# Kernel optimization log

Measured on AMD Instinct MI355X. Metric: run time of the kernel, lower is better.

The kernel has to match this reference:

```python
import jax, jax.numpy as jnp
import numpy as np

N_NODES = 100000
N_EDGES = 1600000
FEAT = 128
EMB = 128
N_ROOTS = 4096


def _gcn_layer(x, W, b, src, dst, n):
    # PyG GCNConv(add_self_loops=False, normalize=False):
    # h = x @ W; out_i = sum_{j in N(i)} h_j ; out = out + bias
    h = x @ W                                  # [N_in, EMB]
    msgs = h[src]                              # gather per edge [E, EMB]
    return jax.ops.segment_sum(msgs, dst, num_segments=n) + b


def setup_inputs() -> dict:
    key = jax.random.key(0)
    k = jax.random.split(key, 10)
    x = jax.random.normal(k[0], (N_NODES, FEAT), dtype=jnp.float32)
    edge_index = jax.random.randint(k[1], (2, N_EDGES), 0, N_NODES, dtype=jnp.int64 if jax.config.jax_enable_x64 else jnp.int32)
    root_mask = jnp.zeros((N_NODES,), dtype=bool).at[:N_ROOTS].set(True)
    s0 = 1.0 / np.sqrt(FEAT)
    s1 = 1.0 / np.sqrt(FEAT + EMB)
    W0 = jax.random.normal(k[2], (FEAT, EMB), dtype=jnp.float32) * s0
    W1 = jax.random.normal(k[3], (EMB + FEAT, EMB), dtype=jnp.float32) * s1
    W2 = jax.random.normal(k[4], (EMB + FEAT, EMB), dtype=jnp.float32) * s1
    W3 = jax.random.normal(k[5], (EMB + FEAT, EMB), dtype=jnp.float32) * s1
    b0 = jnp.zeros((EMB,), jnp.float32)
    b1 = jnp.zeros((EMB,), jnp.float32)
    b2 = jnp.zeros((EMB,), jnp.float32)
    b3 = jnp.zeros((EMB,), jnp.float32)
    return {"x": x, "edge_index": edge_index, "root_mask": root_mask, "num_roots": N_ROOTS,
            "W0": W0, "b0": b0, "W1": W1, "b1": b1, "W2": W2, "b2": b2, "W3": W3, "b3": b3}


def reference(x, edge_index, root_mask, num_roots, W0, b0, W1, b1, W2, b2, W3, b3):
    src, dst = edge_index[0], edge_index[1]
    n = x.shape[0]
    h = _gcn_layer(x, W0, b0, src, dst, n)
    for W, b in ((W1, b1), (W2, b2), (W3, b3)):
        prev = h
        inp = jnp.concatenate((jax.nn.relu(h), x), axis=1)  # concat_initial_features
        h = prev + _gcn_layer(inp, W, b, src, dst, n)        # residual
    roots = jnp.nonzero(root_mask, size=num_roots)[0]
    return h[roots]
```

## Files before the change

kernel.cpp:

```cpp
#include <hip/hip_runtime.h>
#include <hip/hip_bf16.h>
#include <stdint.h>

#define N_NODES 100000
#define N_EDGES 1600000
#define FEAT 128
#define EMB 128
#define N_ROOTS 4096

#define BUCKET_BITS 9
#define BUCKET_NODES 512
#define NBUCK ((N_NODES + BUCKET_NODES - 1) / BUCKET_NODES)
#define BUCK_CAP 12288
#define BIN_CHUNK 4096
#define NB_BIN ((N_EDGES + BIN_CHUNK - 1) / BIN_CHUNK)
#define SRCS_CAP (N_EDGES + N_NODES * 8)

typedef __attribute__((ext_vector_type(4))) float f32x4;
typedef __attribute__((ext_vector_type(8))) short bf16x8;

__device__ __forceinline__ ushort f2b(float f) {
  uint32_t u = __float_as_uint(f);
  uint32_t r = (u + 0x7FFFu + ((u >> 16) & 1u)) >> 16;
  return (ushort)r;
}

__global__ void k_cvt_bf16(const float* __restrict__ in, ushort* __restrict__ out, int n4) {
  int i = blockIdx.x * blockDim.x + threadIdx.x;
  int stride = gridDim.x * blockDim.x;
  for (; i < n4; i += stride) {
    float4 v = ((const float4*)in)[i];
    ushort4 o;
    o.x = f2b(v.x); o.y = f2b(v.y); o.z = f2b(v.z); o.w = f2b(v.w);
    ((ushort4*)out)[i] = o;
  }
}

__global__ __launch_bounds__(256) void k_bin(const int* __restrict__ srcA, const int* __restrict__ dstA,
                                             int* __restrict__ bucket_cnt, int* __restrict__ binned) {
  __shared__ int hist[NBUCK];
  __shared__ int lscan[NBUCK];
  __shared__ int rsv[NBUCK];
  __shared__ int lpos[NBUCK];
  __shared__ int ws[4];
  __shared__ int2 ent[BIN_CHUNK];
  int t = threadIdx.x;
  int e0 = blockIdx.x * BIN_CHUNK;
  int cnt = min(BIN_CHUNK, N_EDGES - e0);
  for (int i = t; i < NBUCK; i += 256) hist[i] = 0;
  __syncthreads();
  for (int j = t; j < cnt; j += 256) atomicAdd(&hist[dstA[e0 + j] >> BUCKET_BITS], 1);
  __syncthreads();
  {
    int lane = t & 63, wv = t >> 6;
    int v = (t < NBUCK) ? hist[t] : 0;
    int inc = v;
    for (int d = 1; d < 64; d <<= 1) { int x = __shfl_up(inc, d); if (lane >= d) inc += x; }
    if (lane == 63) ws[wv] = inc;
    __syncthreads();
    int wbase = 0;
    for (int k = 0; k < wv; ++k) wbase += ws[k];
    if (t < NBUCK) {
      int excl = wbase + inc - v;
      lscan[t] = excl;
      lpos[t] = excl;
      rsv[t] = (v > 0) ? atomicAdd(&bucket_cnt[t], v) : 0;
    }
  }
  __syncthreads();
  for (int j = t; j < cnt; j += 256) {
    int s = srcA[e0 + j], d = dstA[e0 + j];
    int p = atomicAdd(&lpos[d >> BUCKET_BITS], 1);
    ent[p] = make_int2(s, d);
  }
  __syncthreads();
  for (int j = t; j < cnt; j += 256) {
    int2 E = ent[j];
    int b = E.y >> BUCKET_BITS;
    int pos = rsv[b] + (j - lscan[b]);
    if (pos < BUCK_CAP)
      binned[b * BUCK_CAP + pos] = (E.x << BUCKET_BITS) | (E.y & (BUCKET_NODES - 1));
  }
}

__global__ __launch_bounds__(512) void k_deg(const int* __restrict__ binned,
                                             const int* __restrict__ bucket_cnt,
                                             int* __restrict__ degg, int* __restrict__ pad_cnt) {
  __shared__ int deg[BUCKET_NODES];
  __shared__ int ws[8];
  int b = blockIdx.x, t = threadIdx.x;
  int cnt = min(bucket_cnt[b], BUCK_CAP);
  deg[t] = 0;
  __syncthreads();
  for (int j = t; j < cnt; j += 512) atomicAdd(&deg[binned[b * BUCK_CAP + j] & (BUCKET_NODES - 1)], 1);
  __syncthreads();
  int n0 = b * BUCKET_NODES;
  int nn = min(BUCKET_NODES, N_NODES - n0);
  int d = (t < nn) ? deg[t] : 0;
  if (t < nn) degg[n0 + t] = d;
  int dp = (d + 7) & ~7;
  int lane = t & 63, wv = t >> 6;
  for (int q = 1; q < 64; q <<= 1) dp += __shfl_xor(dp, q);
  if (lane == 0) ws[wv] = dp;
  __syncthreads();
  if (t == 0) {
    int tot = 0;
    for (int k = 0; k < 8; ++k) tot += ws[k];
    pad_cnt[b] = tot;
  }
}

__global__ __launch_bounds__(256) void k_bucket_scan(const int* __restrict__ pad_cnt,
                                                     int* __restrict__ bucket_base,
                                                     int* __restrict__ off_last) {
  __shared__ int ws[4];
  int t = threadIdx.x;
  int lane = t & 63, wv = t >> 6;
  int v = (t < NBUCK) ? pad_cnt[t] : 0;
  int inc = v;
  for (int d = 1; d < 64; d <<= 1) { int x = __shfl_up(inc, d); if (lane >= d) inc += x; }
  if (lane == 63) ws[wv] = inc;
  __syncthreads();
  int wbase = 0;
  for (int k = 0; k < wv; ++k) wbase += ws[k];
  if (t < NBUCK) bucket_base[t] = wbase + inc - v;
  if (t == NBUCK - 1) *off_last = wbase + inc;
}

__global__ __launch_bounds__(512) void k_csr(const int* __restrict__ binned,
                                             const int* __restrict__ bucket_cnt,
                                             const int* __restrict__ bucket_base,
                                             const int* __restrict__ degg,
                                             int* __restrict__ off, int* __restrict__ srcs) {
  __shared__ int sAb[BUCKET_NODES];
  __shared__ int sBb[BUCKET_NODES];
  __shared__ int pos[BUCKET_NODES];
  __shared__ int dreal[BUCKET_NODES];
  __shared__ int epk[BUCK_CAP];
  int b = blockIdx.x;
  int t = threadIdx.x;
  int cnt = min(bucket_cnt[b], BUCK_CAP);
  int gbase = bucket_base[b];
  int n0 = b * BUCKET_NODES;
  int nn = min(BUCKET_NODES, N_NODES - n0);
  int d = (t < nn) ? degg[n0 + t] : 0;
  dreal[t] = d;
  int dp = (d + 7) & ~7;
  int* sA = sAb; int* sB = sBb;
  sA[t] = dp;
  __syncthreads();
  for (int q = 1; q < 512; q <<= 1) {
    int x = sA[t];
    if (t >= q) x += sA[t - q];
    sB[t] = x;
    __syncthreads();
    int* tp = sA; sA = sB; sB = tp;
  }
  int ex = sA[t] - dp;
  pos[t] = ex;
  if (t < nn) off[n0 + t] = gbase + ex;
  __syncthreads();
  for (int j = t; j < cnt; j += 512) {
    int p = binned[b * BUCK_CAP + j];
    epk[j] = p;
  }
  __syncthreads();
  for (int j = t; j < cnt; j += 512) {
    int p = epk[j];
    int q = atomicAdd(&pos[p & (BUCKET_NODES - 1)], 1);
    srcs[gbase + q] = p >> BUCKET_BITS;
  }
  __syncthreads();
  int start = sA[t] - dp;
  int fill0 = start + dreal[t];
  int fill1 = start + ((dreal[t] + 7) & ~7);
  for (int q = fill0; q < fill1; ++q) srcs[gbase + q] = N_NODES;
}

__global__ __launch_bounds__(256) void k_gemm(
    const ushort* __restrict__ A0, const ushort* __restrict__ A1,
    const float* __restrict__ W, ushort* __restrict__ out, int n, int K, int relu0)
{
  extern __shared__ char smem[];
  const int KC = K * 128;
  for (int idx = threadIdx.x; idx < KC; idx += 256) {
    int k = idx >> 7, c = idx & 127;
    ushort b = f2b(W[idx]);
    *(ushort*)(smem + c * (K * 2) + ((k * 2) ^ ((c & 7) << 4))) = b;
  }
  __syncthreads();

  int lane = threadIdx.x & 63;
  int wv = threadIdx.x >> 6;
  int rowBase = blockIdx.x * 128 + wv * 32;
  int rl = lane & 15;
  int kh = lane >> 4;
  int r0 = rowBase + rl, r1 = r0 + 16;
  int r0c = min(r0, n - 1), r1c = min(r1, n - 1);

  f32x4 acc[2][8];
#pragma unroll
  for (int i = 0; i < 2; ++i)
#pragma unroll
    for (int j = 0; j < 8; ++j)
      acc[i][j] = (f32x4){0.f, 0.f, 0.f, 0.f};

  int nks = K >> 5;
  for (int ks = 0; ks < nks; ++ks) {
    const ushort* Asrc = (ks < 4) ? A0 : A1;
    int kof = ((ks & 3) << 5) + (kh << 3);
    bf16x8 a0 = *(const bf16x8*)(Asrc + (size_t)r0c * 128 + kof);
    bf16x8 a1 = *(const bf16x8*)(Asrc + (size_t)r1c * 128 + kof);
    if (relu0 && ks < 4) {
#pragma unroll
      for (int q = 0; q < 8; ++q) {
        short v0 = a0[q]; a0[q] = (short)(v0 & ~(v0 >> 15));
        short v1 = a1[q]; a1[q] = (short)(v1 & ~(v1 >> 15));
      }
    }
    int kk = (ks << 5) + (kh << 3);
#pragma unroll
    for (int ct = 0; ct < 8; ++ct) {
      int col = (ct << 4) + rl;
      bf16x8 b = *(const bf16x8*)(smem + col * (K * 2) + ((kk * 2) ^ ((col & 7) << 4)));
      acc[0][ct] = __builtin_amdgcn_mfma_f32_16x16x32_bf16(a0, b, acc[0][ct], 0, 0, 0);
      acc[1][ct] = __builtin_amdgcn_mfma_f32_16x16x32_bf16(a1, b, acc[1][ct], 0, 0, 0);
    }
  }
#pragma unroll
  for (int ri = 0; ri < 2; ++ri)
#pragma unroll
    for (int ct = 0; ct < 8; ++ct) {
      int col = (ct << 4) + rl;
#pragma unroll
      for (int j = 0; j < 4; ++j) {
        int row = rowBase + ri * 16 + kh * 4 + j;
        if (row < n) out[(size_t)row * 128 + col] = f2b(acc[ri][ct][j]);
      }
    }
}

__global__ __launch_bounds__(256) void k_aggr(
    const ushort* __restrict__ hlin, const int* __restrict__ off, const int* __restrict__ srcs,
    const float* __restrict__ bias, ushort* __restrict__ hbf, float* __restrict__ outf,
    int n, int first, int last)
{
  int node = blockIdx.x * 4 + (threadIdx.x >> 6);
  if (node >= n) return;
  int lane = threadIdx.x & 63;
  int s = __builtin_amdgcn_readfirstlane(off[node]);
  int e = __builtin_amdgcn_readfirstlane(off[node + 1]);
  float a0 = 0.f, a1 = 0.f;
  int j = s;
  for (; j + 16 <= e; j += 16) {
    int ix[16];
#pragma unroll
    for (int q = 0; q < 16; ++q) ix[q] = srcs[j + q];
    uint32_t u[16];
#pragma unroll
    for (int q = 0; q < 16; ++q)
      u[q] = *(const uint32_t*)(hlin + (size_t)ix[q] * 128 + lane * 2);
#pragma unroll
    for (int q = 0; q < 16; ++q) {
      a0 += __uint_as_float(u[q] << 16);
      a1 += __uint_as_float(u[q] & 0xFFFF0000u);
    }
  }
  if (j < e) {
    int ix[8];
#pragma unroll
    for (int q = 0; q < 8; ++q) ix[q] = srcs[j + q];
    uint32_t u[8];
#pragma unroll
    for (int q = 0; q < 8; ++q)
      u[q] = *(const uint32_t*)(hlin + (size_t)ix[q] * 128 + lane * 2);
#pragma unroll
    for (int q = 0; q < 8; ++q) {
      a0 += __uint_as_float(u[q] << 16);
      a1 += __uint_as_float(u[q] & 0xFFFF0000u);
    }
  }
  float2 bv = ((const float2*)bias)[lane];
  size_t idx = (size_t)node * 128 + lane * 2;
  float h0, h1;
  if (first) {
    h0 = a0 + bv.x; h1 = a1 + bv.y;
  } else {
    uint32_t up = *(const uint32_t*)(hbf + idx);
    h0 = __uint_as_float(up << 16) + a0 + bv.x;
    h1 = __uint_as_float(up & 0xFFFF0000u) + a1 + bv.y;
  }
  if (last) {
    if (node < N_ROOTS) *(float2*)(outf + idx) = make_float2(h0, h1);
  } else {
    ushort2 r; r.x = f2b(h0); r.y = f2b(h1);
    *(ushort2*)(hbf + idx) = r;
  }
}

extern "C" void kernel_launch(void* const* d_in, const int* in_sizes, int n_in,
                              void* d_out, int out_size, void* d_ws, size_t ws_size,
                              hipStream_t stream) {
  const float* x = (const float*)d_in[0];
  const int* ei  = (const int*)d_in[1];
  const int* src = ei;
  const int* dst = ei + N_EDGES;
  const float* Wp[4] = {(const float*)d_in[4], (const float*)d_in[6],
                        (const float*)d_in[8], (const float*)d_in[10]};
  const float* bp[4] = {(const float*)d_in[5], (const float*)d_in[7],
                        (const float*)d_in[9], (const float*)d_in[11]};

  char* w = (char*)d_ws;
  auto alloc = [&](size_t bytes) {
    char* p = w;
    w += (bytes + 255) & ~(size_t)255;
    return p;
  };
  ushort* x_bf     = (ushort*)alloc((size_t)N_NODES * 128 * 2);
  ushort* hbf      = (ushort*)alloc((size_t)N_NODES * 128 * 2);
  ushort* hlin     = (ushort*)alloc((size_t)(N_NODES + 8) * 128 * 2);
  int*    off      = (int*)   alloc((size_t)(N_NODES + 1) * 4);
  int*    srcs     = (int*)   alloc((size_t)SRCS_CAP * 4);
  int*    binned   = (int*)   alloc((size_t)NBUCK * BUCK_CAP * 4);
  int*    degg     = (int*)   alloc((size_t)N_NODES * 4);
  int*    bucket_cnt  = (int*)alloc((size_t)NBUCK * 4);
  int*    pad_cnt     = (int*)alloc((size_t)NBUCK * 4);
  int*    bucket_base = (int*)alloc((size_t)(NBUCK + 1) * 4);
  if ((size_t)(w - (char*)d_ws) > ws_size) return;

  hipMemsetAsync(bucket_cnt, 0, (size_t)NBUCK * 4, stream);
  hipMemsetAsync(hlin + (size_t)N_NODES * 128, 0, 256, stream);
  k_cvt_bf16<<<2048, 256, 0, stream>>>(x, x_bf, N_NODES * 128 / 4);
  k_bin<<<NB_BIN, 256, 0, stream>>>(src, dst, bucket_cnt, binned);
  k_deg<<<NBUCK, 512, 0, stream>>>(binned, bucket_cnt, degg, pad_cnt);
  k_bucket_scan<<<1, 256, 0, stream>>>(pad_cnt, bucket_base, off + N_NODES);
  k_csr<<<NBUCK, 512, 0, stream>>>(binned, bucket_cnt, bucket_base, degg, off, srcs);

  int gblocks = (N_NODES + 127) / 128;
  int ablocks = (N_NODES + 3) / 4;
  k_gemm<<<gblocks, 256, 128 * 128 * 2, stream>>>(x_bf, x_bf, Wp[0], hlin, N_NODES, 128, 0);
  k_aggr<<<ablocks, 256, 0, stream>>>(hlin, off, srcs, bp[0], hbf, (float*)d_out, N_NODES, 1, 0);
  for (int l = 1; l < 4; ++l) {
    k_gemm<<<gblocks, 256, 256 * 128 * 2, stream>>>(hbf, x_bf, Wp[l], hlin, N_NODES, 256, 1);
    k_aggr<<<ablocks, 256, 0, stream>>>(hlin, off, srcs, bp[l], hbf, (float*)d_out,
                                        N_NODES, 0, (l == 3) ? 1 : 0);
  }
}
```

Before: 403.4 us.

## Slice node features into column slabs and map aggregation slices to XCDs

```diff
diff --git a/kernel.cpp b/kernel.cpp
--- a/kernel.cpp
+++ b/kernel.cpp
@@ -3,10 +3,8 @@
 #include <stdint.h>
 
 #define N_NODES 100000
+#define N_ROOTS 4096
 #define N_EDGES 1600000
-#define FEAT 128
-#define EMB 128
-#define N_ROOTS 4096
 
 #define BUCKET_BITS 9
 #define BUCKET_NODES 512
@@ -14,7 +12,10 @@
 #define BUCK_CAP 12288
 #define BIN_CHUNK 4096
 #define NB_BIN ((N_EDGES + BIN_CHUNK - 1) / BIN_CHUNK)
-#define SRCS_CAP (N_EDGES + N_NODES * 8)
+#define SRCS_CAP (N_EDGES + N_NODES * 8 + 256)
+
+#define ROWSP (N_NODES + 8)
+#define SLABW ((size_t)ROWSP * 32)
 
 typedef __attribute__((ext_vector_type(4))) float f32x4;
 typedef __attribute__((ext_vector_type(8))) short bf16x8;
@@ -25,14 +26,20 @@
   return (ushort)r;
 }
 
-__global__ void k_cvt_bf16(const float* __restrict__ in, ushort* __restrict__ out, int n4) {
-  int i = blockIdx.x * blockDim.x + threadIdx.x;
+__global__ void k_cvt_sliced(const float* __restrict__ in, ushort* __restrict__ out, int n) {
+  int g = blockIdx.x * blockDim.x + threadIdx.x;
   int stride = gridDim.x * blockDim.x;
-  for (; i < n4; i += stride) {
-    float4 v = ((const float4*)in)[i];
-    ushort4 o;
-    o.x = f2b(v.x); o.y = f2b(v.y); o.z = f2b(v.z); o.w = f2b(v.w);
-    ((ushort4*)out)[i] = o;
+  int total = n * 16;
+  for (; g < total; g += stride) {
+    int node = g >> 4, cg = g & 15;
+    const float4* p = (const float4*)(in + (size_t)node * 128 + cg * 8);
+    float4 v0 = p[0], v1 = p[1];
+    uint32_t w0 = (uint32_t)f2b(v0.x) | ((uint32_t)f2b(v0.y) << 16);
+    uint32_t w1 = (uint32_t)f2b(v0.z) | ((uint32_t)f2b(v0.w) << 16);
+    uint32_t w2 = (uint32_t)f2b(v1.x) | ((uint32_t)f2b(v1.y) << 16);
+    uint32_t w3 = (uint32_t)f2b(v1.z) | ((uint32_t)f2b(v1.w) << 16);
+    int slab = cg >> 2, in8 = (cg & 3) * 8;
+    *(uint4*)(out + (size_t)slab * SLABW + (size_t)node * 32 + in8) = make_uint4(w0, w1, w2, w3);
   }
 }
 
@@ -160,10 +167,7 @@
   pos[t] = ex;
   if (t < nn) off[n0 + t] = gbase + ex;
   __syncthreads();
-  for (int j = t; j < cnt; j += 512) {
-    int p = binned[b * BUCK_CAP + j];
-    epk[j] = p;
-  }
+  for (int j = t; j < cnt; j += 512) epk[j] = binned[b * BUCK_CAP + j];
   __syncthreads();
   for (int j = t; j < cnt; j += 512) {
     int p = epk[j];
@@ -209,8 +213,9 @@
   for (int ks = 0; ks < nks; ++ks) {
     const ushort* Asrc = (ks < 4) ? A0 : A1;
     int kof = ((ks & 3) << 5) + (kh << 3);
-    bf16x8 a0 = *(const bf16x8*)(Asrc + (size_t)r0c * 128 + kof);
-    bf16x8 a1 = *(const bf16x8*)(Asrc + (size_t)r1c * 128 + kof);
+    const ushort* ap = Asrc + (size_t)(kof >> 5) * SLABW + (kof & 31);
+    bf16x8 a0 = *(const bf16x8*)(ap + (size_t)r0c * 32);
+    bf16x8 a1 = *(const bf16x8*)(ap + (size_t)r1c * 32);
     if (relu0 && ks < 4) {
 #pragma unroll
       for (int q = 0; q < 8; ++q) {
@@ -231,70 +236,71 @@
   for (int ri = 0; ri < 2; ++ri)
 #pragma unroll
     for (int ct = 0; ct < 8; ++ct) {
-      int col = (ct << 4) + rl;
+      size_t sb = (size_t)(ct >> 1) * SLABW;
+      int incol = ((ct & 1) << 4) + rl;
 #pragma unroll
       for (int j = 0; j < 4; ++j) {
         int row = rowBase + ri * 16 + kh * 4 + j;
-        if (row < n) out[(size_t)row * 128 + col] = f2b(acc[ri][ct][j]);
+        if (row < n) out[sb + (size_t)row * 32 + incol] = f2b(acc[ri][ct][j]);
       }
     }
 }
 
 __global__ __launch_bounds__(256) void k_aggr(
-    const ushort* __restrict__ hlin, const int* __restrict__ off, const int* __restrict__ srcs,
-    const float* __restrict__ bias, ushort* __restrict__ hbf, float* __restrict__ outf,
-    int n, int first, int last)
+    const ushort* __restrict__ hlin_s, const int* __restrict__ off, const int* __restrict__ srcs,
+    const float* __restrict__ bias, ushort* __restrict__ hbf_s, float* __restrict__ outf,
+    int first, int last)
 {
-  int node = blockIdx.x * 4 + (threadIdx.x >> 6);
-  if (node >= n) return;
-  int lane = threadIdx.x & 63;
-  int s = __builtin_amdgcn_readfirstlane(off[node]);
-  int e = __builtin_amdgcn_readfirstlane(off[node + 1]);
+  int b = blockIdx.x;
+  int xcd = b & 7;
+  int slice = xcd >> 1;
+  int half = xcd & 1;
+  int chunk = b >> 3;
+  int lane = threadIdx.x & 63, wv = threadIdx.x >> 6;
+  int ns = lane >> 4, cd = lane & 15;
+  int node = chunk * 32 + half * 16 + wv * 4 + ns;
+  bool valid = node < N_NODES;
+  int s = 0, deg = 0;
+  if (valid) { s = off[node]; deg = off[node + 1] - s; }
+  int dmax = deg;
+  dmax = max(dmax, __shfl_xor(dmax, 16));
+  dmax = max(dmax, __shfl_xor(dmax, 32));
+  const uint32_t* slab = (const uint32_t*)hlin_s + (size_t)slice * (SLABW / 2);
   float a0 = 0.f, a1 = 0.f;
-  int j = s;
-  for (; j + 16 <= e; j += 16) {
-    int ix[16];
-#pragma unroll
-    for (int q = 0; q < 16; ++q) ix[q] = srcs[j + q];
-    uint32_t u[16];
-#pragma unroll
-    for (int q = 0; q < 16; ++q)
-      u[q] = *(const uint32_t*)(hlin + (size_t)ix[q] * 128 + lane * 2);
-#pragma unroll
-    for (int q = 0; q < 16; ++q) {
-      a0 += __uint_as_float(u[q] << 16);
-      a1 += __uint_as_float(u[q] & 0xFFFF0000u);
-    }
-  }
-  if (j < e) {
-    int ix[8];
-#pragma unroll
-    for (int q = 0; q < 8; ++q) ix[q] = srcs[j + q];
+  for (int j = 0; j < dmax; j += 8) {
+    bool live = (j < deg);
+    int idx[8];
+#pragma unroll
+    for (int q = 0; q < 8; ++q) {
+      int ii = srcs[s + j + q];
+      idx[q] = live ? ii : N_NODES;
+    }
     uint32_t u[8];
 #pragma unroll
-    for (int q = 0; q < 8; ++q)
-      u[q] = *(const uint32_t*)(hlin + (size_t)ix[q] * 128 + lane * 2);
+    for (int q = 0; q < 8; ++q) u[q] = slab[(size_t)idx[q] * 16 + cd];
 #pragma unroll
     for (int q = 0; q < 8; ++q) {
       a0 += __uint_as_float(u[q] << 16);
       a1 += __uint_as_float(u[q] & 0xFFFF0000u);
     }
   }
-  float2 bv = ((const float2*)bias)[lane];
-  size_t idx = (size_t)node * 128 + lane * 2;
+  if (!valid) return;
+  float2 bv = ((const float2*)bias)[slice * 16 + cd];
+  uint32_t* hb = (uint32_t*)hbf_s + (size_t)slice * (SLABW / 2);
+  size_t hi = (size_t)node * 16 + cd;
   float h0, h1;
   if (first) {
     h0 = a0 + bv.x; h1 = a1 + bv.y;
   } else {
-    uint32_t up = *(const uint32_t*)(hbf + idx);
+    uint32_t up = hb[hi];
     h0 = __uint_as_float(up << 16) + a0 + bv.x;
     h1 = __uint_as_float(up & 0xFFFF0000u) + a1 + bv.y;
   }
   if (last) {
-    if (node < N_ROOTS) *(float2*)(outf + idx) = make_float2(h0, h1);
+    if (node < N_ROOTS)
+      *(float2*)(outf + (size_t)node * 128 + slice * 32 + cd * 2) = make_float2(h0, h1);
   } else {
-    ushort2 r; r.x = f2b(h0); r.y = f2b(h1);
-    *(ushort2*)(hbf + idx) = r;
+    hb[hi] = (uint32_t)f2b(h0) | ((uint32_t)f2b(h1) << 16);
   }
 }
 
@@ -316,9 +322,9 @@
     w += (bytes + 255) & ~(size_t)255;
     return p;
   };
-  ushort* x_bf     = (ushort*)alloc((size_t)N_NODES * 128 * 2);
-  ushort* hbf      = (ushort*)alloc((size_t)N_NODES * 128 * 2);
-  ushort* hlin     = (ushort*)alloc((size_t)(N_NODES + 8) * 128 * 2);
+  ushort* xs       = (ushort*)alloc(4 * SLABW * 2);
+  ushort* hbf_s    = (ushort*)alloc(4 * SLABW * 2);
+  ushort* hlin_s   = (ushort*)alloc(4 * SLABW * 2);
   int*    off      = (int*)   alloc((size_t)(N_NODES + 1) * 4);
   int*    srcs     = (int*)   alloc((size_t)SRCS_CAP * 4);
   int*    binned   = (int*)   alloc((size_t)NBUCK * BUCK_CAP * 4);
@@ -329,20 +335,21 @@
   if ((size_t)(w - (char*)d_ws) > ws_size) return;
 
   hipMemsetAsync(bucket_cnt, 0, (size_t)NBUCK * 4, stream);
-  hipMemsetAsync(hlin + (size_t)N_NODES * 128, 0, 256, stream);
-  k_cvt_bf16<<<2048, 256, 0, stream>>>(x, x_bf, N_NODES * 128 / 4);
+  for (int sl = 0; sl < 4; ++sl)
+    hipMemsetAsync(hlin_s + (size_t)sl * SLABW + (size_t)N_NODES * 32, 0, 64, stream);
+  k_cvt_sliced<<<2048, 256, 0, stream>>>(x, xs, N_NODES);
   k_bin<<<NB_BIN, 256, 0, stream>>>(src, dst, bucket_cnt, binned);
   k_deg<<<NBUCK, 512, 0, stream>>>(binned, bucket_cnt, degg, pad_cnt);
   k_bucket_scan<<<1, 256, 0, stream>>>(pad_cnt, bucket_base, off + N_NODES);
   k_csr<<<NBUCK, 512, 0, stream>>>(binned, bucket_cnt, bucket_base, degg, off, srcs);
 
   int gblocks = (N_NODES + 127) / 128;
-  int ablocks = (N_NODES + 3) / 4;
-  k_gemm<<<gblocks, 256, 128 * 128 * 2, stream>>>(x_bf, x_bf, Wp[0], hlin, N_NODES, 128, 0);
-  k_aggr<<<ablocks, 256, 0, stream>>>(hlin, off, srcs, bp[0], hbf, (float*)d_out, N_NODES, 1, 0);
+  int ablocks = ((N_NODES + 31) / 32) * 8;
+  k_gemm<<<gblocks, 256, 128 * 128 * 2, stream>>>(xs, xs, Wp[0], hlin_s, N_NODES, 128, 0);
+  k_aggr<<<ablocks, 256, 0, stream>>>(hlin_s, off, srcs, bp[0], hbf_s, (float*)d_out, 1, 0);
   for (int l = 1; l < 4; ++l) {
-    k_gemm<<<gblocks, 256, 256 * 128 * 2, stream>>>(hbf, x_bf, Wp[l], hlin, N_NODES, 256, 1);
-    k_aggr<<<ablocks, 256, 0, stream>>>(hlin, off, srcs, bp[l], hbf, (float*)d_out,
-                                        N_NODES, 0, (l == 3) ? 1 : 0);
-  }
-}
+    k_gemm<<<gblocks, 256, 256 * 128 * 2, stream>>>(hbf_s, xs, Wp[l], hlin_s, N_NODES, 256, 1);
+    k_aggr<<<ablocks, 256, 0, stream>>>(hlin_s, off, srcs, bp[l], hbf_s, (float*)d_out,
+                                        0, (l == 3) ? 1 : 0);
+  }
+}
```

New measurement: 441.2 us. 1.09x slower.

## Process two nodes per wave in aggregation and limit final layer to roots

Applied to the files above, without the earlier changes.

```diff
diff --git a/kernel.cpp b/kernel.cpp
--- a/kernel.cpp
+++ b/kernel.cpp
@@ -14,7 +14,7 @@
 #define BUCK_CAP 12288
 #define BIN_CHUNK 4096
 #define NB_BIN ((N_EDGES + BIN_CHUNK - 1) / BIN_CHUNK)
-#define SRCS_CAP (N_EDGES + N_NODES * 8)
+#define SRCS_CAP (N_EDGES + N_NODES * 8 + 256)
 
 typedef __attribute__((ext_vector_type(4))) float f32x4;
 typedef __attribute__((ext_vector_type(8))) short bf16x8;
@@ -160,10 +160,7 @@
   pos[t] = ex;
   if (t < nn) off[n0 + t] = gbase + ex;
   __syncthreads();
-  for (int j = t; j < cnt; j += 512) {
-    int p = binned[b * BUCK_CAP + j];
-    epk[j] = p;
-  }
+  for (int j = t; j < cnt; j += 512) epk[j] = binned[b * BUCK_CAP + j];
   __syncthreads();
   for (int j = t; j < cnt; j += 512) {
     int p = epk[j];
@@ -245,56 +242,115 @@
     const float* __restrict__ bias, ushort* __restrict__ hbf, float* __restrict__ outf,
     int n, int first, int last)
 {
-  int node = blockIdx.x * 4 + (threadIdx.x >> 6);
-  if (node >= n) return;
+  int wv = threadIdx.x >> 6;
   int lane = threadIdx.x & 63;
-  int s = __builtin_amdgcn_readfirstlane(off[node]);
-  int e = __builtin_amdgcn_readfirstlane(off[node + 1]);
-  float a0 = 0.f, a1 = 0.f;
-  int j = s;
-  for (; j + 16 <= e; j += 16) {
-    int ix[16];
-#pragma unroll
-    for (int q = 0; q < 16; ++q) ix[q] = srcs[j + q];
+  int nodeA = blockIdx.x * 8 + wv * 2;
+  if (nodeA >= n) return;
+  int nodeB = nodeA + 1;
+  bool hasB = nodeB < n;
+  int sA = __builtin_amdgcn_readfirstlane(off[nodeA]);
+  int eA = __builtin_amdgcn_readfirstlane(off[nodeA + 1]);
+  int eB = hasB ? __builtin_amdgcn_readfirstlane(off[nodeB + 1]) : eA;
+  float aA0 = 0.f, aA1 = 0.f, aB0 = 0.f, aB1 = 0.f;
+  int ja = sA, jb = eA;
+  while (ja + 8 <= eA && jb + 8 <= eB) {
+    int4 pa0 = *(const int4*)(srcs + ja), pa1 = *(const int4*)(srcs + ja + 4);
+    int4 pb0 = *(const int4*)(srcs + jb), pb1 = *(const int4*)(srcs + jb + 4);
     uint32_t u[16];
-#pragma unroll
-    for (int q = 0; q < 16; ++q)
-      u[q] = *(const uint32_t*)(hlin + (size_t)ix[q] * 128 + lane * 2);
-#pragma unroll
-    for (int q = 0; q < 16; ++q) {
-      a0 += __uint_as_float(u[q] << 16);
-      a1 += __uint_as_float(u[q] & 0xFFFF0000u);
-    }
-  }
-  if (j < e) {
-    int ix[8];
-#pragma unroll
-    for (int q = 0; q < 8; ++q) ix[q] = srcs[j + q];
+    u[0]  = *(const uint32_t*)(hlin + (size_t)pa0.x * 128 + lane * 2);
+    u[1]  = *(const uint32_t*)(hlin + (size_t)pa0.y * 128 + lane * 2);
+    u[2]  = *(const uint32_t*)(hlin + (size_t)pa0.z * 128 + lane * 2);
+    u[3]  = *(const uint32_t*)(hlin + (size_t)pa0.w * 128 + lane * 2);
+    u[4]  = *(const uint32_t*)(hlin + (size_t)pa1.x * 128 + lane * 2);
+    u[5]  = *(const uint32_t*)(hlin + (size_t)pa1.y * 128 + lane * 2);
+    u[6]  = *(const uint32_t*)(hlin + (size_t)pa1.z * 128 + lane * 2);
+    u[7]  = *(const uint32_t*)(hlin + (size_t)pa1.w * 128 + lane * 2);
+    u[8]  = *(const uint32_t*)(hlin + (size_t)pb0.x * 128 + lane * 2);
+    u[9]  = *(const uint32_t*)(hlin + (size_t)pb0.y * 128 + lane * 2);
+    u[10] = *(const uint32_t*)(hlin + (size_t)pb0.z * 128 + lane * 2);
+    u[11] = *(const uint32_t*)(hlin + (size_t)pb0.w * 128 + lane * 2);
+    u[12] = *(const uint32_t*)(hlin + (size_t)pb1.x * 128 + lane * 2);
+    u[13] = *(const uint32_t*)(hlin + (size_t)pb1.y * 128 + lane * 2);
+    u[14] = *(const uint32_t*)(hlin + (size_t)pb1.z * 128 + lane * 2);
+    u[15] = *(const uint32_t*)(hlin + (size_t)pb1.w * 128 + lane * 2);
+#pragma unroll
+    for (int q = 0; q < 8; ++q) {
+      aA0 += __uint_as_float(u[q] << 16);
+      aA1 += __uint_as_float(u[q] & 0xFFFF0000u);
+    }
+#pragma unroll
+    for (int q = 8; q < 16; ++q) {
+      aB0 += __uint_as_float(u[q] << 16);
+      aB1 += __uint_as_float(u[q] & 0xFFFF0000u);
+    }
+    ja += 8; jb += 8;
+  }
+  for (; ja + 8 <= eA; ja += 8) {
+    int4 p0 = *(const int4*)(srcs + ja), p1 = *(const int4*)(srcs + ja + 4);
     uint32_t u[8];
-#pragma unroll
-    for (int q = 0; q < 8; ++q)
-      u[q] = *(const uint32_t*)(hlin + (size_t)ix[q] * 128 + lane * 2);
+    u[0] = *(const uint32_t*)(hlin + (size_t)p0.x * 128 + lane * 2);
+    u[1] = *(const uint32_t*)(hlin + (size_t)p0.y * 128 + lane * 2);
+    u[2] = *(const uint32_t*)(hlin + (size_t)p0.z * 128 + lane * 2);
+    u[3] = *(const uint32_t*)(hlin + (size_t)p0.w * 128 + lane * 2);
+    u[4] = *(const uint32_t*)(hlin + (size_t)p1.x * 128 + lane * 2);
+    u[5] = *(const uint32_t*)(hlin + (size_t)p1.y * 128 + lane * 2);
+    u[6] = *(const uint32_t*)(hlin + (size_t)p1.z * 128 + lane * 2);
+    u[7] = *(const uint32_t*)(hlin + (size_t)p1.w * 128 + lane * 2);
 #pragma unroll
     for (int q = 0; q < 8; ++q) {
-      a0 += __uint_as_float(u[q] << 16);
-      a1 += __uint_as_float(u[q] & 0xFFFF0000u);
+      aA0 += __uint_as_float(u[q] << 16);
+      aA1 += __uint_as_float(u[q] & 0xFFFF0000u);
+    }
+  }
+  for (; jb + 8 <= eB; jb += 8) {
+    int4 p0 = *(const int4*)(srcs + jb), p1 = *(const int4*)(srcs + jb + 4);
+    uint32_t u[8];
+    u[0] = *(const uint32_t*)(hlin + (size_t)p0.x * 128 + lane * 2);
+    u[1] = *(const uint32_t*)(hlin + (size_t)p0.y * 128 + lane * 2);
+    u[2] = *(const uint32_t*)(hlin + (size_t)p0.z * 128 + lane * 2);
+    u[3] = *(const uint32_t*)(hlin + (size_t)p0.w * 128 + lane * 2);
+    u[4] = *(const uint32_t*)(hlin + (size_t)p1.x * 128 + lane * 2);
+    u[5] = *(const uint32_t*)(hlin + (size_t)p1.y * 128 + lane * 2);
+    u[6] = *(const uint32_t*)(hlin + (size_t)p1.z * 128 + lane * 2);
+    u[7] = *(const uint32_t*)(hlin + (size_t)p1.w * 128 + lane * 2);
+#pragma unroll
+    for (int q = 0; q < 8; ++q) {
+      aB0 += __uint_as_float(u[q] << 16);
+      aB1 += __uint_as_float(u[q] & 0xFFFF0000u);
     }
   }
   float2 bv = ((const float2*)bias)[lane];
-  size_t idx = (size_t)node * 128 + lane * 2;
-  float h0, h1;
-  if (first) {
-    h0 = a0 + bv.x; h1 = a1 + bv.y;
-  } else {
-    uint32_t up = *(const uint32_t*)(hbf + idx);
-    h0 = __uint_as_float(up << 16) + a0 + bv.x;
-    h1 = __uint_as_float(up & 0xFFFF0000u) + a1 + bv.y;
-  }
-  if (last) {
-    if (node < N_ROOTS) *(float2*)(outf + idx) = make_float2(h0, h1);
-  } else {
-    ushort2 r; r.x = f2b(h0); r.y = f2b(h1);
-    *(ushort2*)(hbf + idx) = r;
+  {
+    size_t idx = (size_t)nodeA * 128 + lane * 2;
+    float h0, h1;
+    if (first) { h0 = aA0 + bv.x; h1 = aA1 + bv.y; }
+    else {
+      uint32_t up = *(const uint32_t*)(hbf + idx);
+      h0 = __uint_as_float(up << 16) + aA0 + bv.x;
+      h1 = __uint_as_float(up & 0xFFFF0000u) + aA1 + bv.y;
+    }
+    if (last) {
+      *(float2*)(outf + idx) = make_float2(h0, h1);
+    } else {
+      ushort2 r; r.x = f2b(h0); r.y = f2b(h1);
+      *(ushort2*)(hbf + idx) = r;
+    }
+  }
+  if (hasB) {
+    size_t idx = (size_t)nodeB * 128 + lane * 2;
+    float h0, h1;
+    if (first) { h0 = aB0 + bv.x; h1 = aB1 + bv.y; }
+    else {
+      uint32_t up = *(const uint32_t*)(hbf + idx);
+      h0 = __uint_as_float(up << 16) + aB0 + bv.x;
+      h1 = __uint_as_float(up & 0xFFFF0000u) + aB1 + bv.y;
+    }
+    if (last) {
+      *(float2*)(outf + idx) = make_float2(h0, h1);
+    } else {
+      ushort2 r; r.x = f2b(h0); r.y = f2b(h1);
+      *(ushort2*)(hbf + idx) = r;
+    }
   }
 }
 
@@ -337,12 +393,17 @@
   k_csr<<<NBUCK, 512, 0, stream>>>(binned, bucket_cnt, bucket_base, degg, off, srcs);
 
   int gblocks = (N_NODES + 127) / 128;
-  int ablocks = (N_NODES + 3) / 4;
+  int ablocks = (N_NODES + 7) / 8;
   k_gemm<<<gblocks, 256, 128 * 128 * 2, stream>>>(x_bf, x_bf, Wp[0], hlin, N_NODES, 128, 0);
   k_aggr<<<ablocks, 256, 0, stream>>>(hlin, off, srcs, bp[0], hbf, (float*)d_out, N_NODES, 1, 0);
   for (int l = 1; l < 4; ++l) {
     k_gemm<<<gblocks, 256, 256 * 128 * 2, stream>>>(hbf, x_bf, Wp[l], hlin, N_NODES, 256, 1);
-    k_aggr<<<ablocks, 256, 0, stream>>>(hlin, off, srcs, bp[l], hbf, (float*)d_out,
-                                        N_NODES, 0, (l == 3) ? 1 : 0);
-  }
-}
+    if (l < 3) {
+      k_aggr<<<ablocks, 256, 0, stream>>>(hlin, off, srcs, bp[l], hbf, (float*)d_out,
+                                          N_NODES, 0, 0);
+    } else {
+      k_aggr<<<(N_ROOTS + 7) / 8, 256, 0, stream>>>(hlin, off, srcs, bp[l], hbf, (float*)d_out,
+                                                    N_ROOTS, 0, 1);
+    }
+  }
+}
```

Measured after the change: 356.1 us. -11.7%, faster.
